# Kernel tuning notes

Hardware: AMD Instinct MI355X
Metric: run time of the kernel (lower is better)

## Reference

```python
import jax, jax.numpy as jnp
import numpy as np

B, S, D = 2, 2048, 4096
NH, NKV = 32, 8
HD = D // NH          # 128
NREP = NH // NKV      # 4
THETA = 10000.0


def _rope_tables(seq_len, head_dim):
    inv = 1.0 / (THETA ** (jnp.arange(0, head_dim, 2, dtype=jnp.float32) / head_dim))  # [HD/2]
    t = jnp.arange(seq_len, dtype=jnp.float32)
    ang = jnp.outer(t, inv)                      # [S, HD/2]
    return jnp.cos(ang), jnp.sin(ang)


def _apply_rope(x, cos, sin):
    # x: [b, s, h, d]; interleaved pairs (even=real, odd=imag), matching view_as_complex
    xr = x.reshape(*x.shape[:-1], HD // 2, 2)
    x0, x1 = xr[..., 0], xr[..., 1]
    c = cos[None, :, None, :]
    s = sin[None, :, None, :]
    o0 = x0 * c - x1 * s
    o1 = x0 * s + x1 * c
    return jnp.stack([o0, o1], axis=-1).reshape(x.shape)


def setup_inputs() -> dict:
    key = jax.random.key(0)
    ks = jax.random.split(key, 5)
    sc = 0.02
    return {
        "x": jax.random.normal(ks[0], (B, S, D), jnp.float32),
        "wq": jax.random.normal(ks[1], (D, NH * HD), jnp.float32) * sc,
        "wk": jax.random.normal(ks[2], (D, NKV * HD), jnp.float32) * sc,
        "wv": jax.random.normal(ks[3], (D, NKV * HD), jnp.float32) * sc,
        "wo": jax.random.normal(ks[4], (NH * HD, D), jnp.float32) * sc,
        "start_pos": 0,
        "inference": 0,
    }


def reference(x, wq, wk, wv, wo, start_pos, inference):
    bsz, seq_len, _ = x.shape
    # QKV projections (training path: inference=False)
    xq = (x @ wq).reshape(bsz, seq_len, NH, HD)
    xk = (x @ wk).reshape(bsz, seq_len, NKV, HD)
    xv = (x @ wv).reshape(bsz, seq_len, NKV, HD)

    cos, sin = _rope_tables(seq_len, HD)
    xq = _apply_rope(xq, cos, sin)
    xk = _apply_rope(xk, cos, sin)

    # GQA without materializing repeated KV: group q heads per kv head
    q = xq.reshape(bsz, seq_len, NKV, NREP, HD)           # [b, s, g, r, d]
    scores = jnp.einsum('bqgrd,bkgd->bgrqk', q, xk) / np.sqrt(HD)
    causal = jnp.triu(jnp.full((seq_len, seq_len), -jnp.inf, jnp.float32), k=1)
    scores = scores + causal
    probs = jax.nn.softmax(scores.astype(jnp.float32), axis=-1).astype(x.dtype)
    out = jnp.einsum('bgrqk,bkgd->bqgrd', probs, xv)      # [b, s, g, r, d]
    out = out.reshape(bsz, seq_len, NH * HD)
    return out @ wo
```

## Files before the change

kernel.cpp:

```cpp
#include <hip/hip_runtime.h>
#include <hip/hip_bf16.h>

#define B_ 2
#define S_ 2048
#define D_ 4096
#define NH_ 32
#define NKV_ 8
#define HD_ 128
#define NREP_ 4

typedef unsigned short u16;
typedef __attribute__((ext_vector_type(8))) short short8;
typedef __attribute__((ext_vector_type(4))) float f32x4;

__device__ inline float bf2f(u16 u) {
    union { unsigned u; float f; } v; v.u = ((unsigned)u) << 16; return v.f;
}
__device__ inline u16 f2bf(float f) {
    union { float f; unsigned u; } v; v.f = f;
    unsigned r = v.u + 0x7fffu + ((v.u >> 16) & 1u);
    return (u16)(r >> 16);
}
__device__ inline unsigned cvt_pk(float lo, float hi) {
    unsigned r;
    asm("v_cvt_pk_bf16_f32 %0, %1, %2" : "=v"(r) : "v"(lo), "v"(hi));
    return r;
}
__device__ inline float exp2_fast(float x) {
    float r;
    asm("v_exp_f32 %0, %1" : "=v"(r) : "v"(x));
    return r;
}

__device__ inline void gl_lds16(const u16* g, u16* l) {
    __builtin_amdgcn_global_load_lds(
        (const __attribute__((address_space(1))) unsigned int*)g,
        (__attribute__((address_space(3))) unsigned int*)l, 16, 0, 0);
}

__global__ __launch_bounds__(256) void conv_k(const float* __restrict__ in,
                                              u16* __restrict__ out) {
    size_t i = ((size_t)blockIdx.x * 256 + threadIdx.x) * 4;
    float4 v = *(const float4*)&in[i];
    uint2 t;
    t.x = cvt_pk(v.x, v.y);
    t.y = cvt_pk(v.z, v.w);
    *(uint2*)&out[i] = t;
}

__global__ __launch_bounds__(256) void tconv_k(const float* __restrict__ in,
                                               u16* __restrict__ out,
                                               int R, int C) {
    __shared__ u16 tile[64][65];
    int bx = blockIdx.x * 64, by = blockIdx.y * 64;
    int tx = threadIdx.x, ty = threadIdx.y;
    for (int i = ty; i < 64; i += 4)
        tile[i][tx] = f2bf(in[(size_t)(by + i) * C + bx + tx]);
    __syncthreads();
    for (int i = ty; i < 64; i += 4)
        out[(size_t)(bx + i) * R + by + tx] = tile[tx][i];
}

__global__ __launch_bounds__(256) void tconv2_k(const float* __restrict__ in0,
                                                const float* __restrict__ in1,
                                                u16* __restrict__ out0,
                                                u16* __restrict__ out1,
                                                int R, int C) {
    __shared__ u16 tile[64][65];
    const float* in = blockIdx.z ? in1 : in0;
    u16* out = blockIdx.z ? out1 : out0;
    int bx = blockIdx.x * 64, by = blockIdx.y * 64;
    int tx = threadIdx.x, ty = threadIdx.y;
    for (int i = ty; i < 64; i += 4)
        tile[i][tx] = f2bf(in[(size_t)(by + i) * C + bx + tx]);
    __syncthreads();
    for (int i = ty; i < 64; i += 4)
        out[(size_t)(bx + i) * R + by + tx] = tile[tx][i];
}

__global__ __launch_bounds__(256) void transpose_k(const u16* __restrict__ in,
                                                   u16* __restrict__ out,
                                                   int R, int C) {
    __shared__ u16 tile[64][65];
    const u16* ib = in + (size_t)blockIdx.z * R * C;
    u16* ob = out + (size_t)blockIdx.z * R * C;
    int bx = blockIdx.x * 64, by = blockIdx.y * 64;
    int tx = threadIdx.x, ty = threadIdx.y;
    for (int i = ty; i < 64; i += 4)
        tile[i][tx] = ib[(size_t)(by + i) * C + bx + tx];
    __syncthreads();
    for (int i = ty; i < 64; i += 4)
        ob[(size_t)(bx + i) * R + by + tx] = tile[tx][i];
}


__device__ inline short8 lds_frag(const u16* base, int row, int colb) {
    int off = ((row >> 7) << 14) + ((row & 127) << 7) + (colb ^ ((row & 7) << 4));
    return *(const short8*)((const char*)base + off);
}

__device__ inline void stage_half(const u16* g, int row0, int ldK, int k0,
                                  u16* ldsHalf, int w, int lane) {
#pragma unroll
    for (int j = 0; j < 2; ++j) {
        int Lb = (w << 11) + (j << 10) + (lane << 4);
        int r  = Lb >> 7;
        int c  = (Lb & 127) ^ ((r & 7) << 4);
        const u16* gp = g + (size_t)(row0 + r) * ldK + k0 + (c >> 1);
        gl_lds16(gp, ldsHalf + (((w << 11) + (j << 10)) >> 1));
    }
}

#define PH_MFMA(MB)                                                           \
    asm volatile("s_waitcnt lgkmcnt(0)" ::: "memory");                        \
    __builtin_amdgcn_sched_barrier(0);                                        \
    __builtin_amdgcn_s_setprio(1);                                            \
    _Pragma("unroll") for (int mi = 0; mi < 2; ++mi)                          \
      _Pragma("unroll") for (int ni = 0; ni < 4; ++ni)                        \
        _Pragma("unroll") for (int kk = 0; kk < 2; ++kk)                      \
          acc[(MB) + mi][ni] = __builtin_amdgcn_mfma_f32_16x16x32_bf16(       \
              af[mi][kk], bfr[ni][kk], acc[(MB) + mi][ni], 0, 0, 0);          \
    __builtin_amdgcn_s_setprio(0);                                            \
    __builtin_amdgcn_s_barrier();

#define TILE_BODY(T, CURA, CURB, OTHA)                                        \
  {                                                                           \
    const int t_ = (T);                                                       \
    const bool p1_ = (t_ + 1 < nt), p2_ = (t_ + 2 < nt);                      \
    short8 bfr[4][2], af[2][2];                                               \
    _Pragma("unroll") for (int ni = 0; ni < 4; ++ni)                          \
      _Pragma("unroll") for (int kk = 0; kk < 2; ++kk)                        \
        bfr[ni][kk] = lds_frag(CURB, wn * 64 + ni * 16 + ln, kk * 64 + qd * 16); \
    _Pragma("unroll") for (int mi = 0; mi < 2; ++mi)                          \
      _Pragma("unroll") for (int kk = 0; kk < 2; ++kk)                        \
        af[mi][kk] = lds_frag(CURA, wm * 128 + mi * 16 + ln, kk * 64 + qd * 16); \
    if (p1_) stage_half(Ag, 0, K, (t_ + 1) << 6, OTHA, w, lane);              \
    asm volatile("s_waitcnt lgkmcnt(8)" ::: "memory");                        \
    __builtin_amdgcn_s_barrier();                                             \
    PH_MFMA(0)                                                                \
    _Pragma("unroll") for (int mi = 0; mi < 2; ++mi)                          \
      _Pragma("unroll") for (int kk = 0; kk < 2; ++kk)                        \
        af[mi][kk] = lds_frag(CURA, wm * 128 + (mi + 2) * 16 + ln, kk * 64 + qd * 16); \
    if (p1_) stage_half(Ag, 128, K, (t_ + 1) << 6, OTHA + 8192, w, lane);     \
    __builtin_amdgcn_s_barrier();                                             \
    PH_MFMA(2)                                                                \
    _Pragma("unroll") for (int mi = 0; mi < 2; ++mi)                          \
      _Pragma("unroll") for (int kk = 0; kk < 2; ++kk)                        \
        af[mi][kk] = lds_frag(CURA, wm * 128 + (mi + 4) * 16 + ln, kk * 64 + qd * 16); \
    if (p2_) stage_half(Bg, 0, K, (t_ + 2) << 6, CURB, w, lane);              \
    __builtin_amdgcn_s_barrier();                                             \
    PH_MFMA(4)                                                                \
    _Pragma("unroll") for (int mi = 0; mi < 2; ++mi)                          \
      _Pragma("unroll") for (int kk = 0; kk < 2; ++kk)                        \
        af[mi][kk] = lds_frag(CURA, wm * 128 + (mi + 6) * 16 + ln, kk * 64 + qd * 16); \
    if (p2_) {                                                                \
        stage_half(Bg, 128, K, (t_ + 2) << 6, CURB + 8192, w, lane);          \
        asm volatile("s_waitcnt vmcnt(4)" ::: "memory");                      \
    } else if (p1_) {                                                         \
        asm volatile("s_waitcnt vmcnt(0)" ::: "memory");                      \
    }                                                                         \
    __builtin_amdgcn_s_barrier();                                             \
    PH_MFMA(6)                                                                \
  }

template <int OUT_MODE>
__global__ __launch_bounds__(512, 1) void gemm256(const u16* __restrict__ A,
                                                  const u16* __restrict__ Bt,
                                                  void* __restrict__ Cv,
                                                  int M, int N, int K) {
    __shared__ __align__(16) u16 As[2][16384];
    __shared__ __align__(16) u16 Bs[2][16384];

    int tid = threadIdx.x;
    int w = tid >> 6, lane = tid & 63;
    int ln = lane & 15, qd = lane >> 4;
    int wm = w >> 2, wn = w & 3;

    int nbx = N >> 8;
    int cpx = gridDim.x >> 3;
    int bid = blockIdx.x;
    int swz = (bid & 7) * cpx + (bid >> 3);
    int m0 = (swz / nbx) << 8;
    int n0 = (swz % nbx) << 8;

    const u16* Ag = A + (size_t)m0 * K;
    const u16* Bg = Bt + (size_t)n0 * K;
    int nt = K >> 6;

    f32x4 acc[8][4];
#pragma unroll
    for (int i = 0; i < 8; ++i)
#pragma unroll
        for (int j = 0; j < 4; ++j) acc[i][j] = f32x4{0.f, 0.f, 0.f, 0.f};

    u16* A0 = &As[0][0]; u16* A1v = &As[1][0];
    u16* B0 = &Bs[0][0]; u16* B1v = &Bs[1][0];

    stage_half(Ag, 0,   K, 0,  A0,         w, lane);
    stage_half(Ag, 128, K, 0,  A0 + 8192,  w, lane);
    stage_half(Bg, 0,   K, 0,  B0,         w, lane);
    stage_half(Bg, 128, K, 0,  B0 + 8192,  w, lane);
    stage_half(Bg, 0,   K, 64, B1v,        w, lane);
    stage_half(Bg, 128, K, 64, B1v + 8192, w, lane);
    asm volatile("s_waitcnt vmcnt(4)" ::: "memory");
    __builtin_amdgcn_s_barrier();

    for (int tt = 0; tt < nt; tt += 2) {
        TILE_BODY(tt,     A0,  B0,  A1v)
        TILE_BODY(tt + 1, A1v, B1v, A0)
    }

#pragma unroll
    for (int mi = 0; mi < 8; ++mi)
#pragma unroll
        for (int ni = 0; ni < 4; ++ni)
#pragma unroll
            for (int r = 0; r < 4; ++r) {
                int row = m0 + wm * 128 + mi * 16 + qd * 4 + r;
                int col = n0 + wn * 64 + ni * 16 + ln;
                if (OUT_MODE == 1)
                    ((float*)Cv)[(size_t)row * N + col] = acc[mi][ni][r];
                else if (OUT_MODE == 0)
                    ((u16*)Cv)[(size_t)row * N + col] = f2bf(acc[mi][ni][r]);
                else {
                    u16* dst = (u16*)Cv + ((col < 1024) ? 0 : (4096ull * 1024 - 1024));
                    dst[(size_t)row * 1024 + col] = f2bf(acc[mi][ni][r]);
                }
            }
}

__global__ __launch_bounds__(256) void rope_k(u16* __restrict__ Q,
                                              u16* __restrict__ Kb,
                                              float qscale) {
    const int ngq = B_ * S_ * NH_ * (HD_ / 8);
    const int ngk = B_ * S_ * NKV_ * (HD_ / 8);
    int i = blockIdx.x * 256 + threadIdx.x;
    u16* buf; int nheads; float scale;
    if (i < ngq) { buf = Q; nheads = NH_; scale = qscale; }
    else {
        i -= ngq;
        if (i >= ngk) return;
        buf = Kb; nheads = NKV_; scale = 1.f;
    }
    int gp = i & 15;
    int hh = (i >> 4) % nheads;
    int row = i / (16 * nheads);
    int s = row & (S_ - 1);
    size_t base = ((size_t)row * nheads + hh) * HD_ + gp * 8;
    uint4 v = *(const uint4*)&buf[base];
    unsigned ov[4];
    unsigned* vp = (unsigned*)&v;
#pragma unroll
    for (int j = 0; j < 4; ++j) {
        int p = gp * 4 + j;
        float freq = __expf(-(float)(2 * p) * (9.210340371976184f / 128.0f));
        float ang = (float)s * freq;
        float c, sn;
        sincosf(ang, &sn, &c);
        float x0 = bf2f((u16)vp[j]), x1 = bf2f((u16)(vp[j] >> 16));
        ov[j] = cvt_pk((x0 * c - x1 * sn) * scale, (x0 * sn + x1 * c) * scale);
    }
    *(uint4*)&buf[base] = *(uint4*)ov;
}

__global__ __launch_bounds__(512, 4) void attn_k(const u16* __restrict__ Q,
                                                 const u16* __restrict__ K,
                                                 const u16* __restrict__ Vt,
                                                 u16* __restrict__ AO) {
    __shared__ __align__(16) u16 Ks[2][64 * 128];
    __shared__ __align__(16) u16 Vts[2][128 * 64];

    int tid = threadIdx.x;
    int w = tid >> 6, lane = tid & 63;
    int ln = lane & 15, qd = lane >> 4;
    int sw = (ln & 7) << 4;

    int h  = blockIdx.y;
    int b  = blockIdx.z;
    int g  = h >> 2;

    const u16* Kbase = K + (size_t)(b * S_) * (NKV_ * HD_) + g * HD_;
    const u16* Vtb   = Vt + ((size_t)(b * NKV_ + g)) * HD_ * S_;

    int kr0 = tid >> 4;
    int kg0 = (tid & 15) * 8;
    int kcs = (kg0 * 2) ^ ((kr0 & 7) << 4);
    int vr0 = tid >> 3;
    int vg0 = (tid & 7) * 8;
    int vcs = (vg0 * 2) ^ ((vr0 & 7) << 4);

    for (int pass = 0; pass < 2; ++pass) {
        int qt = pass ? (S_ / 128 - 1 - (int)blockIdx.x) : (int)blockIdx.x;
        int q0 = qt * 128;
        int qb = q0 + w * 16;
        int qg = qb + ln;
        int ntw   = ((qb + 15) >> 6) + 1;
        int nfull = (qb + 1) >> 6;

        const u16* qptr = Q + ((size_t)(b * S_ + qg)) * (NH_ * HD_) + h * HD_;
        short8 bq[4];
#pragma unroll
        for (int kq = 0; kq < 4; ++kq)
            bq[kq] = *(const short8*)(qptr + kq * 32 + qd * 8);

        f32x4 ot[8];
#pragma unroll
        for (int db = 0; db < 8; ++db) ot[db] = f32x4{0.f, 0.f, 0.f, 0.f};
        float m_s = -1e30f, l_s = 0.f;

        int nk = 2 * qt + 2;

        {
            int4 a0 = *(const int4*)(Kbase + (size_t)kr0 * (NKV_ * HD_) + kg0);
            int4 a1 = *(const int4*)(Kbase + (size_t)(kr0 + 32) * (NKV_ * HD_) + kg0);
            int4 v0 = *(const int4*)(Vtb + (size_t)vr0 * S_ + vg0);
            int4 v1 = *(const int4*)(Vtb + (size_t)(vr0 + 64) * S_ + vg0);
            *(int4*)((char*)&Ks[0][0] + kr0 * 256 + kcs) = a0;
            *(int4*)((char*)&Ks[0][0] + (kr0 + 32) * 256 + kcs) = a1;
            *(int4*)((char*)&Vts[0][0] + vr0 * 128 + vcs) = v0;
            *(int4*)((char*)&Vts[0][0] + (vr0 + 64) * 128 + vcs) = v1;
        }
        __syncthreads();

        for (int kt = 0; kt < nk; ++kt) {
            int bb = kt & 1;
            int k0 = kt * 64;
            bool pf = (kt + 1 < nk);
            int4 pa0, pa1, pv0, pv1;
            if (pf) {
                int k0n = k0 + 64;
                pa0 = *(const int4*)(Kbase + (size_t)(k0n + kr0) * (NKV_ * HD_) + kg0);
                pa1 = *(const int4*)(Kbase + (size_t)(k0n + kr0 + 32) * (NKV_ * HD_) + kg0);
                pv0 = *(const int4*)(Vtb + (size_t)vr0 * S_ + k0n + vg0);
                pv1 = *(const int4*)(Vtb + (size_t)(vr0 + 64) * S_ + k0n + vg0);
            }

            if (kt < ntw) {
                f32x4 st[4];
#pragma unroll
                for (int kb = 0; kb < 4; ++kb) st[kb] = f32x4{0.f, 0.f, 0.f, 0.f};
                __builtin_amdgcn_s_setprio(1);
#pragma unroll
                for (int kb = 0; kb < 4; ++kb)
#pragma unroll
                    for (int kq = 0; kq < 4; ++kq) {
                        short8 ak = *(const short8*)((const char*)&Ks[bb][0] +
                                    (kb * 16 + ln) * 256 + ((kq * 64 + qd * 16) ^ sw));
                        st[kb] = __builtin_amdgcn_mfma_f32_16x16x32_bf16(ak, bq[kq], st[kb], 0, 0, 0);
                    }
                __builtin_amdgcn_s_setprio(0);

                float mx;
                if (kt >= nfull) {
                    int lim = qg - k0 - qd * 4;
                    mx = -1e30f;
#pragma unroll
                    for (int kb = 0; kb < 4; ++kb)
#pragma unroll
                        for (int r = 0; r < 4; ++r) {
                            if (16 * kb + r > lim) st[kb][r] = -1e30f;
                            mx = fmaxf(mx, st[kb][r]);
                        }
                } else {
                    mx = st[0][0];
#pragma unroll
                    for (int kb = 0; kb < 4; ++kb)
#pragma unroll
                        for (int r = 0; r < 4; ++r)
                            if (kb + r) mx = fmaxf(mx, st[kb][r]);
                }
                mx = fmaxf(mx, __shfl_xor(mx, 16, 64));
                mx = fmaxf(mx, __shfl_xor(mx, 32, 64));

                if (__any(mx > m_s + 8.f)) {
                    float mn = fmaxf(m_s, mx);
                    float alpha = exp2_fast(m_s - mn);
                    m_s = mn;
                    l_s *= alpha;
#pragma unroll
                    for (int db = 0; db < 8; ++db)
#pragma unroll
                        for (int r = 0; r < 4; ++r) ot[db][r] *= alpha;
                }
                float rs = 0.f;
#pragma unroll
                for (int kb = 0; kb < 4; ++kb)
#pragma unroll
                    for (int r = 0; r < 4; ++r) {
                        float pv = exp2_fast(st[kb][r] - m_s);
                        st[kb][r] = pv;
                        rs += pv;
                    }
                rs += __shfl_xor(rs, 16, 64);
                rs += __shfl_xor(rs, 32, 64);
                l_s += rs;

                unsigned pk[4][2];
#pragma unroll
                for (int kb = 0; kb < 4; ++kb) {
                    pk[kb][0] = cvt_pk(st[kb][0], st[kb][1]);
                    pk[kb][1] = cvt_pk(st[kb][2], st[kb][3]);
                }
                int sA = ((qd & 1) << 5) + ln;
                int sB = sA + 16;
                bool hi = (qd & 2) != 0;
#pragma unroll
                for (int ks = 0; ks < 2; ++ks) {
                    unsigned t0a = (unsigned)__shfl((int)pk[2 * ks][0], sA, 64);
                    unsigned t0b = (unsigned)__shfl((int)pk[2 * ks][1], sA, 64);
                    unsigned t1a = (unsigned)__shfl((int)pk[2 * ks + 1][0], sA, 64);
                    unsigned t1b = (unsigned)__shfl((int)pk[2 * ks + 1][1], sA, 64);
                    unsigned t2a = (unsigned)__shfl((int)pk[2 * ks][0], sB, 64);
                    unsigned t2b = (unsigned)__shfl((int)pk[2 * ks][1], sB, 64);
                    unsigned t3a = (unsigned)__shfl((int)pk[2 * ks + 1][0], sB, 64);
                    unsigned t3b = (unsigned)__shfl((int)pk[2 * ks + 1][1], sB, 64);
                    union { unsigned u[4]; short8 s8; } bp;
                    bp.u[0] = hi ? t1a : t0a;
                    bp.u[1] = hi ? t1b : t0b;
                    bp.u[2] = hi ? t3a : t2a;
                    bp.u[3] = hi ? t3b : t2b;
                    __builtin_amdgcn_s_setprio(1);
#pragma unroll
                    for (int db = 0; db < 8; ++db) {
                        short8 av = *(const short8*)((const char*)&Vts[bb][0] +
                                    (db * 16 + ln) * 128 + ((ks * 64 + qd * 16) ^ sw));
                        ot[db] = __builtin_amdgcn_mfma_f32_16x16x32_bf16(av, bp.s8, ot[db], 0, 0, 0);
                    }
                    __builtin_amdgcn_s_setprio(0);
                }
            }

            if (pf) {
                int nb2 = bb ^ 1;
                *(int4*)((char*)&Ks[nb2][0] + kr0 * 256 + kcs) = pa0;
                *(int4*)((char*)&Ks[nb2][0] + (kr0 + 32) * 256 + kcs) = pa1;
                *(int4*)((char*)&Vts[nb2][0] + vr0 * 128 + vcs) = pv0;
                *(int4*)((char*)&Vts[nb2][0] + (vr0 + 64) * 128 + vcs) = pv1;
            }
            __syncthreads();
        }

        float invl = 1.0f / l_s;
        size_t orow = (size_t)(b * S_ + qg) * (NH_ * HD_) + h * HD_;
#pragma unroll
        for (int db = 0; db < 8; ++db) {
            uint2 t2;
            t2.x = cvt_pk(ot[db][0] * invl, ot[db][1] * invl);
            t2.y = cvt_pk(ot[db][2] * invl, ot[db][3] * invl);
            *(uint2*)&AO[orow + db * 16 + qd * 4] = t2;
        }
    }
}

extern "C" void kernel_launch(void* const* d_in, const int* in_sizes, int n_in,
                              void* d_out, int out_size, void* d_ws, size_t ws_size,
                              hipStream_t stream) {
    const float* x  = (const float*)d_in[0];
    const float* wq = (const float*)d_in[1];
    const float* wk = (const float*)d_in[2];
    const float* wv = (const float*)d_in[3];
    const float* wo = (const float*)d_in[4];
    float* out = (float*)d_out;

    char* p = (char*)d_ws;
    auto alloc = [&](size_t nelem) { u16* r = (u16*)p; p += nelem * 2; return r; };
    u16* xb  = alloc(4096ull * 4096);
    u16* wqT = alloc(4096ull * 4096);
    u16* wkT = alloc(1024ull * 4096);
    u16* wvT = alloc(1024ull * 4096);
    u16* Q   = alloc(4096ull * 4096);
    u16* Kb  = alloc(4096ull * 1024);
    u16* Vb  = alloc(4096ull * 1024);
    u16* AO  = alloc(4096ull * 4096);

    dim3 tblk(64, 4);
    conv_k<<<16384, 256, 0, stream>>>(x, xb);
    tconv_k<<<dim3(64, 64), tblk, 0, stream>>>(wq, wqT, 4096, 4096);
    tconv2_k<<<dim3(16, 64, 2), tblk, 0, stream>>>(wk, wv, wkT, wvT, 4096, 1024);

    gemm256<0><<<256, 512, 0, stream>>>(xb, wqT, Q, 4096, 4096, 4096);
    gemm256<2><<<128, 512, 0, stream>>>(xb, wkT, Kb, 4096, 2048, 4096);

    u16* woT = xb;
    u16* Vt  = wqT;
    tconv_k<<<dim3(64, 64), tblk, 0, stream>>>(wo, woT, 4096, 4096);

    int ng = B_ * S_ * NH_ * (HD_ / 8) + B_ * S_ * NKV_ * (HD_ / 8);
    rope_k<<<(ng + 255) / 256, 256, 0, stream>>>(Q, Kb, 0.12751743f);

    transpose_k<<<dim3(16, 32, 2), tblk, 0, stream>>>(Vb, Vt, S_, NKV_ * HD_);

    attn_k<<<dim3(S_ / 256, NH_, B_), 512, 0, stream>>>(Q, Kb, Vt, AO);

    gemm256<1><<<256, 512, 0, stream>>>(AO, woT, out, 4096, 4096, 4096);
}
```

Before: 724.7 us.

## Run GEMM with 16 waves per block, halving per-wave M tile

```diff
diff --git a/kernel.cpp b/kernel.cpp
--- a/kernel.cpp
+++ b/kernel.cpp
@@ -101,25 +101,20 @@
 
 __device__ inline void stage_half(const u16* g, int row0, int ldK, int k0,
                                   u16* ldsHalf, int w, int lane) {
-#pragma unroll
-    for (int j = 0; j < 2; ++j) {
-        int Lb = (w << 11) + (j << 10) + (lane << 4);
-        int r  = Lb >> 7;
-        int c  = (Lb & 127) ^ ((r & 7) << 4);
-        const u16* gp = g + (size_t)(row0 + r) * ldK + k0 + (c >> 1);
-        gl_lds16(gp, ldsHalf + (((w << 11) + (j << 10)) >> 1));
-    }
-}
-
-#define PH_MFMA(MB)                                                           \
+    int Lb = (w << 10) + (lane << 4);
+    int r  = Lb >> 7;
+    int c  = (Lb & 127) ^ ((r & 7) << 4);
+    gl_lds16(g + (size_t)(row0 + r) * ldK + k0 + (c >> 1), ldsHalf + (w << 9));
+}
+
+#define PH_MFMA(KK)                                                           \
     asm volatile("s_waitcnt lgkmcnt(0)" ::: "memory");                        \
     __builtin_amdgcn_sched_barrier(0);                                        \
     __builtin_amdgcn_s_setprio(1);                                            \
-    _Pragma("unroll") for (int mi = 0; mi < 2; ++mi)                          \
+    _Pragma("unroll") for (int mi = 0; mi < 4; ++mi)                          \
       _Pragma("unroll") for (int ni = 0; ni < 4; ++ni)                        \
-        _Pragma("unroll") for (int kk = 0; kk < 2; ++kk)                      \
-          acc[(MB) + mi][ni] = __builtin_amdgcn_mfma_f32_16x16x32_bf16(       \
-              af[mi][kk], bfr[ni][kk], acc[(MB) + mi][ni], 0, 0, 0);          \
+          acc[mi][ni] = __builtin_amdgcn_mfma_f32_16x16x32_bf16(              \
+              af[mi], bfr[ni][KK], acc[mi][ni], 0, 0, 0);                     \
     __builtin_amdgcn_s_setprio(0);                                            \
     __builtin_amdgcn_s_barrier();
 
@@ -127,47 +122,39 @@
   {                                                                           \
     const int t_ = (T);                                                       \
     const bool p1_ = (t_ + 1 < nt), p2_ = (t_ + 2 < nt);                      \
-    short8 bfr[4][2], af[2][2];                                               \
+    short8 bfr[4][2], af[4];                                                  \
+                       \
     _Pragma("unroll") for (int ni = 0; ni < 4; ++ni)                          \
       _Pragma("unroll") for (int kk = 0; kk < 2; ++kk)                        \
         bfr[ni][kk] = lds_frag(CURB, wn * 64 + ni * 16 + ln, kk * 64 + qd * 16); \
-    _Pragma("unroll") for (int mi = 0; mi < 2; ++mi)                          \
-      _Pragma("unroll") for (int kk = 0; kk < 2; ++kk)                        \
-        af[mi][kk] = lds_frag(CURA, wm * 128 + mi * 16 + ln, kk * 64 + qd * 16); \
-    if (p1_) stage_half(Ag, 0, K, (t_ + 1) << 6, OTHA, w, lane);              \
+    _Pragma("unroll") for (int mi = 0; mi < 4; ++mi)                          \
+        af[mi] = lds_frag(CURA, wm * 64 + mi * 16 + ln, qd * 16);             \
+    if (p1_) {                                                                \
+        stage_half(Ag, 0,   K, (t_ + 1) << 6, OTHA,        w, lane);          \
+        stage_half(Ag, 128, K, (t_ + 1) << 6, OTHA + 8192, w, lane);          \
+    }                                                                         \
     asm volatile("s_waitcnt lgkmcnt(8)" ::: "memory");                        \
     __builtin_amdgcn_s_barrier();                                             \
     PH_MFMA(0)                                                                \
-    _Pragma("unroll") for (int mi = 0; mi < 2; ++mi)                          \
-      _Pragma("unroll") for (int kk = 0; kk < 2; ++kk)                        \
-        af[mi][kk] = lds_frag(CURA, wm * 128 + (mi + 2) * 16 + ln, kk * 64 + qd * 16); \
-    if (p1_) stage_half(Ag, 128, K, (t_ + 1) << 6, OTHA + 8192, w, lane);     \
-    __builtin_amdgcn_s_barrier();                                             \
-    PH_MFMA(2)                                                                \
-    _Pragma("unroll") for (int mi = 0; mi < 2; ++mi)                          \
-      _Pragma("unroll") for (int kk = 0; kk < 2; ++kk)                        \
-        af[mi][kk] = lds_frag(CURA, wm * 128 + (mi + 4) * 16 + ln, kk * 64 + qd * 16); \
-    if (p2_) stage_half(Bg, 0, K, (t_ + 2) << 6, CURB, w, lane);              \
-    __builtin_amdgcn_s_barrier();                                             \
-    PH_MFMA(4)                                                                \
-    _Pragma("unroll") for (int mi = 0; mi < 2; ++mi)                          \
-      _Pragma("unroll") for (int kk = 0; kk < 2; ++kk)                        \
-        af[mi][kk] = lds_frag(CURA, wm * 128 + (mi + 6) * 16 + ln, kk * 64 + qd * 16); \
+                            \
+    _Pragma("unroll") for (int mi = 0; mi < 4; ++mi)                          \
+        af[mi] = lds_frag(CURA, wm * 64 + mi * 16 + ln, 64 + qd * 16);        \
     if (p2_) {                                                                \
+        stage_half(Bg, 0,   K, (t_ + 2) << 6, CURB,        w, lane);          \
         stage_half(Bg, 128, K, (t_ + 2) << 6, CURB + 8192, w, lane);          \
-        asm volatile("s_waitcnt vmcnt(4)" ::: "memory");                      \
+        asm volatile("s_waitcnt vmcnt(2)" ::: "memory");                      \
     } else if (p1_) {                                                         \
         asm volatile("s_waitcnt vmcnt(0)" ::: "memory");                      \
     }                                                                         \
     __builtin_amdgcn_s_barrier();                                             \
-    PH_MFMA(6)                                                                \
+    PH_MFMA(1)                                                                \
   }
 
 template <int OUT_MODE>
-__global__ __launch_bounds__(512, 1) void gemm256(const u16* __restrict__ A,
-                                                  const u16* __restrict__ Bt,
-                                                  void* __restrict__ Cv,
-                                                  int M, int N, int K) {
+__global__ __launch_bounds__(1024, 1) void gemm256(const u16* __restrict__ A,
+                                                   const u16* __restrict__ Bt,
+                                                   void* __restrict__ Cv,
+                                                   int M, int N, int K) {
     __shared__ __align__(16) u16 As[2][16384];
     __shared__ __align__(16) u16 Bs[2][16384];
 
@@ -187,9 +174,9 @@
     const u16* Bg = Bt + (size_t)n0 * K;
     int nt = K >> 6;
 
-    f32x4 acc[8][4];
-#pragma unroll
-    for (int i = 0; i < 8; ++i)
+    f32x4 acc[4][4];
+#pragma unroll
+    for (int i = 0; i < 4; ++i)
 #pragma unroll
         for (int j = 0; j < 4; ++j) acc[i][j] = f32x4{0.f, 0.f, 0.f, 0.f};
 
@@ -202,7 +189,7 @@
     stage_half(Bg, 128, K, 0,  B0 + 8192,  w, lane);
     stage_half(Bg, 0,   K, 64, B1v,        w, lane);
     stage_half(Bg, 128, K, 64, B1v + 8192, w, lane);
-    asm volatile("s_waitcnt vmcnt(4)" ::: "memory");
+    asm volatile("s_waitcnt vmcnt(2)" ::: "memory");
     __builtin_amdgcn_s_barrier();
 
     for (int tt = 0; tt < nt; tt += 2) {
@@ -211,12 +198,12 @@
     }
 
 #pragma unroll
-    for (int mi = 0; mi < 8; ++mi)
+    for (int mi = 0; mi < 4; ++mi)
 #pragma unroll
         for (int ni = 0; ni < 4; ++ni)
 #pragma unroll
             for (int r = 0; r < 4; ++r) {
-                int row = m0 + wm * 128 + mi * 16 + qd * 4 + r;
+                int row = m0 + wm * 64 + mi * 16 + qd * 4 + r;
                 int col = n0 + wn * 64 + ni * 16 + ln;
                 if (OUT_MODE == 1)
                     ((float*)Cv)[(size_t)row * N + col] = acc[mi][ni][r];
@@ -478,8 +465,8 @@
     tconv_k<<<dim3(64, 64), tblk, 0, stream>>>(wq, wqT, 4096, 4096);
     tconv2_k<<<dim3(16, 64, 2), tblk, 0, stream>>>(wk, wv, wkT, wvT, 4096, 1024);
 
-    gemm256<0><<<256, 512, 0, stream>>>(xb, wqT, Q, 4096, 4096, 4096);
-    gemm256<2><<<128, 512, 0, stream>>>(xb, wkT, Kb, 4096, 2048, 4096);
+    gemm256<0><<<256, 1024, 0, stream>>>(xb, wqT, Q, 4096, 4096, 4096);
+    gemm256<2><<<128, 1024, 0, stream>>>(xb, wkT, Kb, 4096, 2048, 4096);
 
     u16* woT = xb;
     u16* Vt  = wqT;
@@ -492,5 +479,5 @@
 
     attn_k<<<dim3(S_ / 256, NH_, B_), 512, 0, stream>>>(Q, Kb, Vt, AO);
 
-    gemm256<1><<<256, 512, 0, stream>>>(AO, woT, out, 4096, 4096, 4096);
-}
+    gemm256<1><<<256, 1024, 0, stream>>>(AO, woT, out, 4096, 4096, 4096);
+}
```

New measurement: 1.017 ms. 40.3% more time.
